# Optimization experiments

Measured on AMD Instinct MI355X. Metric: run time of the kernel, lower is better.

## Reference

```python
import jax, jax.numpy as jnp
import numpy as np

C = 64
C8 = C // 8
C16 = C // 16


def setup_inputs() -> dict:
    key = jax.random.key(0)
    ks = jax.random.split(key, 11)
    s = lambda fan_in: 1.0 / np.sqrt(fan_in)
    return {
        "x": jax.random.normal(ks[0], (4, C, 64, 64), dtype=jnp.float32),
        # 1x1 convs == per-pixel linear: weight [out, in], bias [out]
        "Wq": jax.random.uniform(ks[1], (C8, C), minval=-s(C), maxval=s(C)),
        "bq": jax.random.uniform(ks[2], (C8,), minval=-s(C), maxval=s(C)),
        "Wk": jax.random.uniform(ks[3], (C8, C), minval=-s(C), maxval=s(C)),
        "bk": jax.random.uniform(ks[4], (C8,), minval=-s(C), maxval=s(C)),
        "Wv": jax.random.uniform(ks[5], (C, C), minval=-s(C), maxval=s(C)),
        "bv": jax.random.uniform(ks[6], (C,), minval=-s(C), maxval=s(C)),
        "W1": jax.random.uniform(ks[7], (C16, C), minval=-s(C), maxval=s(C)),
        "b1": jax.random.uniform(ks[8], (C16,), minval=-s(C), maxval=s(C)),
        "W2": jax.random.uniform(ks[9], (C, C16), minval=-s(C16), maxval=s(C16)),
        "b2": jax.random.uniform(ks[10], (C,), minval=-s(C16), maxval=s(C16)),
    }


def reference(x, Wq, bq, Wk, bk, Wv, bv, W1, b1, W2, b2):
    b, c, h, w = x.shape
    n = h * w
    xf = x.reshape(b, c, n)                                   # [b,c,n]
    Q = jnp.einsum('qc,bcn->bnq', Wq, xf) + bq                # [b,n,c/8]
    K = jnp.einsum('kc,bcn->bkn', Wk, xf) + bk[None, :, None] # [b,c/8,n]
    V = jnp.einsum('vc,bcn->bvn', Wv, xf) + bv[None, :, None] # [b,c,n]
    scores = jnp.einsum('bnq,bqm->bnm', Q, K) / jnp.sqrt(jnp.float32(c))
    att = jax.nn.softmax(scores, axis=-1)                     # [b,n,n]
    # self_attention_map = V @ att^T
    sa = jnp.einsum('bvm,bnm->bvn', V, att).reshape(b, c, h, w)
    # SE-style channel gate
    avg = xf.mean(axis=2)                                     # [b,c]
    gate = jax.nn.sigmoid(jax.nn.relu(avg @ W1.T + b1) @ W2.T + b2)
    return sa * gate[:, :, None, None]
```

## Files before the change

### kernel.cpp

```cpp
#include <hip/hip_runtime.h>
#include <hip/hip_bf16.h>

typedef __attribute__((ext_vector_type(8))) short bf16x8;
typedef __attribute__((ext_vector_type(4))) float f32x4;
typedef __attribute__((ext_vector_type(4))) unsigned short u16x4;
typedef __attribute__((ext_vector_type(8))) unsigned short u16x8;

#define WS_QB 0
#define WS_KB 131072
#define WS_VB 262144
#define WS_AVG_U 1310720

__device__ __forceinline__ unsigned short bf_hi(float x) {
    __hip_bfloat16 h = __float2bfloat16(x);
    return *reinterpret_cast<unsigned short*>(&h);
}
__device__ __forceinline__ unsigned int bfpk(float lo, float hi) {
    return (unsigned int)bf_hi(lo) | ((unsigned int)bf_hi(hi) << 16);
}

__global__ __launch_bounds__(256) void proj_kernel(
    const float* __restrict__ x,
    const float* __restrict__ Wq, const float* __restrict__ bq,
    const float* __restrict__ Wk, const float* __restrict__ bk,
    const float* __restrict__ Wv, const float* __restrict__ bv,
    unsigned short* __restrict__ Qb, unsigned short* __restrict__ Kb,
    unsigned short* __restrict__ Vb, float* __restrict__ avg)
{
    __shared__ __align__(16) unsigned short Wls[16 * 72];

    const int tid = threadIdx.x;
    const int w = tid >> 6;
    const int l = tid & 63;
    const int g = l >> 4;
    const int l15 = l & 15;

    const int tile = blockIdx.x >> 8;
    const int pair = blockIdx.x & 255;
    const int b = pair >> 6;
    const int n0 = (pair & 63) << 6;
    const int n = n0 + w * 16 + l15;
    const float* xb = x + b * 262144;

    float xr[2][8];
#pragma unroll
    for (int kcb = 0; kcb < 2; ++kcb)
#pragma unroll
        for (int j = 0; j < 8; ++j)
            xr[kcb][j] = xb[(kcb * 32 + g * 8 + j) * 4096 + n];

#pragma unroll
    for (int i = 0; i < 4; ++i) {
        const int idx = i * 256 + tid;
        const int row = idx >> 6, col = idx & 63;
        float wv;
        if (tile == 0) wv = (row < 8) ? Wq[row * 64 + col] : Wk[(row - 8) * 64 + col];
        else           wv = Wv[((tile - 1) * 16 + row) * 64 + col];
        Wls[row * 72 + col] = bf_hi(wv);
    }
    __syncthreads();

    bf16x8 bfr[2];
#pragma unroll
    for (int kcb = 0; kcb < 2; ++kcb)
#pragma unroll
        for (int j = 0; j < 8; ++j)
            bfr[kcb][j] = (short)bf_hi(xr[kcb][j]);

    const bf16x8 a0 = *(const bf16x8*)&Wls[l15 * 72 + g * 8];
    const bf16x8 a1 = *(const bf16x8*)&Wls[l15 * 72 + 32 + g * 8];
    f32x4 acc;
#pragma unroll
    for (int r = 0; r < 4; ++r) acc[r] = 0.0f;
    acc = __builtin_amdgcn_mfma_f32_16x16x32_bf16(a0, bfr[0], acc, 0, 0, 0);
    acc = __builtin_amdgcn_mfma_f32_16x16x32_bf16(a1, bfr[1], acc, 0, 0, 0);

    if (tile == 0) {
        u16x4 ov;
        if (g < 2) {
#pragma unroll
            for (int r = 0; r < 4; ++r) ov[r] = bf_hi((acc[r] + bq[g * 4 + r]) * 0.125f);
            *(u16x4*)&Qb[(b * 4096 + n) * 8 + g * 4] = ov;
        } else {
#pragma unroll
            for (int r = 0; r < 4; ++r) ov[r] = bf_hi(acc[r] + bk[(g - 2) * 4 + r]);
            *(u16x4*)&Kb[(b * 4096 + n) * 8 + (g - 2) * 4] = ov;
        }
        const int c = tid >> 2;
        const float* xrow = xb + c * 4096 + n0 + ((tid & 3) << 4);
        float s = 0.0f;
#pragma unroll
        for (int k = 0; k < 4; ++k) {
            const float4 v = *(const float4*)&xrow[k * 4];
            s += (v.x + v.y) + (v.z + v.w);
        }
        s += __shfl_xor(s, 1);
        s += __shfl_xor(s, 2);
        if ((tid & 3) == 0) atomicAdd(&avg[b * 64 + c], s * (1.0f / 4096.0f));
    } else {
#pragma unroll
        for (int r = 0; r < 4; ++r) {
            const int v = (tile - 1) * 16 + g * 4 + r;
            Vb[(b * 64 + v) * 4096 + n] = bf_hi(acc[r] + bv[v]);
        }
    }
}

__global__ __launch_bounds__(512, 4) void attn_kernel(
    const unsigned short* __restrict__ Qb, const unsigned short* __restrict__ Kb,
    const unsigned short* __restrict__ Vb, const float* __restrict__ avg,
    const float* __restrict__ W1, const float* __restrict__ b1,
    const float* __restrict__ W2, const float* __restrict__ b2,
    float* __restrict__ out)
{
    __shared__ float osum[4][64][33];
    __shared__ float zls[32], gls[64], avgs[64];

    const int t = threadIdx.x;
    const int w = t >> 6;
    const int l = t & 63;
    const int g = l >> 4;
    const int l15 = l & 15;
    const int godd = g & 1;
    const int gs = (godd << 1) | (g >> 1);

    const int wg = (blockIdx.x & 7) * 64 + (blockIdx.x >> 3);
    const int b = wg >> 7;
    const int q0 = (wg & 127) << 5;

    if (t < 32) zls[t] = 0.0f;
    if (t < 64) avgs[t] = avg[b * 64 + t];
    __syncthreads();

    bf16x8 zf = {};
    bf16x8 qf[2];
#pragma unroll
    for (int qt = 0; qt < 2; ++qt) {
        bf16x8 v = *(const bf16x8*)&Qb[(b * 4096 + q0 + qt * 16 + l15) * 8];
        qf[qt] = (g == 0) ? v : zf;
    }

    const unsigned short* kb = Kb + b * 4096 * 8;
    const unsigned short* vbB = Vb + (b * 64) * 4096;

    int m0 = w * 32;
    bf16x8 kpa = zf, kpb = zf;
    if (g == 0) {
        kpa = *(const bf16x8*)&kb[(m0 + l15) * 8];
        kpb = *(const bf16x8*)&kb[(m0 + 16 + l15) * 8];
    }
    bf16x8 vp[4];
#pragma unroll
    for (int vt = 0; vt < 4; ++vt)
        vp[vt] = *(const bf16x8*)&vbB[(vt * 16 + l15) * 4096 + m0 + gs * 8];

    f32x4 acc[2][4];
#pragma unroll
    for (int qt = 0; qt < 2; ++qt)
#pragma unroll
        for (int vt = 0; vt < 4; ++vt)
#pragma unroll
            for (int r = 0; r < 4; ++r) acc[qt][vt][r] = 0.0f;
    float zreg[2] = {0.f, 0.f};

    for (int ci = 0; ci < 16; ++ci) {
        const bf16x8 ka = kpa, kc = kpb;
        bf16x8 vc[4];
#pragma unroll
        for (int vt = 0; vt < 4; ++vt) vc[vt] = vp[vt];

        const int m0n = (ci < 15) ? (w + 8 * (ci + 1)) * 32 : m0;
        if (g == 0) {
            kpa = *(const bf16x8*)&kb[(m0n + l15) * 8];
            kpb = *(const bf16x8*)&kb[(m0n + 16 + l15) * 8];
        }
#pragma unroll
        for (int vt = 0; vt < 4; ++vt)
            vp[vt] = *(const bf16x8*)&vbB[(vt * 16 + l15) * 4096 + m0n + gs * 8];

        f32x4 dz;
#pragma unroll
        for (int r = 0; r < 4; ++r) dz[r] = 0.0f;

        bf16x8 bp[2];
#pragma unroll
        for (int qt = 0; qt < 2; ++qt) {
            f32x4 d0 = __builtin_amdgcn_mfma_f32_16x16x32_bf16(ka, qf[qt], dz, 0, 0, 0);
            f32x4 d1 = __builtin_amdgcn_mfma_f32_16x16x32_bf16(kc, qf[qt], dz, 0, 0, 0);
            float p0[4], p1[4];
#pragma unroll
            for (int r = 0; r < 4; ++r) { p0[r] = __expf(d0[r]); p1[r] = __expf(d1[r]); }
            zreg[qt] += ((p0[0] + p0[1]) + (p0[2] + p0[3]))
                      + ((p1[0] + p1[1]) + (p1[2] + p1[3]));
            const unsigned int A = bfpk(p0[0], p0[1]), B = bfpk(p0[2], p0[3]);
            const unsigned int C = bfpk(p1[0], p1[1]), D = bfpk(p1[2], p1[3]);
            const unsigned int s1 = godd ? A : C;
            const unsigned int s2 = godd ? B : D;
            const unsigned int r1 = __shfl_xor(s1, 16);
            const unsigned int r2 = __shfl_xor(s2, 16);
            union { unsigned int u[4]; bf16x8 v; } pw;
            pw.u[0] = godd ? r1 : A;
            pw.u[1] = godd ? r2 : B;
            pw.u[2] = godd ? C : r1;
            pw.u[3] = godd ? D : r2;
            bp[qt] = pw.v;
        }

        __builtin_amdgcn_s_setprio(1);
#pragma unroll
        for (int vt = 0; vt < 4; ++vt) {
            acc[0][vt] = __builtin_amdgcn_mfma_f32_16x16x32_bf16(vc[vt], bp[0], acc[0][vt], 0, 0, 0);
            acc[1][vt] = __builtin_amdgcn_mfma_f32_16x16x32_bf16(vc[vt], bp[1], acc[1][vt], 0, 0, 0);
        }
        __builtin_amdgcn_s_setprio(0);
        m0 = m0n;
    }

#pragma unroll
    for (int qt = 0; qt < 2; ++qt) {
        float z = zreg[qt];
        z += __shfl_xor(z, 16);
        z += __shfl_xor(z, 32);
        if (g == 0) atomicAdd(&zls[qt * 16 + l15], z);
    }

    if (w < 4) {
#pragma unroll
        for (int qt = 0; qt < 2; ++qt)
#pragma unroll
            for (int vt = 0; vt < 4; ++vt)
#pragma unroll
                for (int r = 0; r < 4; ++r)
                    osum[w][vt * 16 + g * 4 + r][qt * 16 + l15] = acc[qt][vt][r];
    }
    if (t < 64) {
        float hreg[4];
#pragma unroll
        for (int j = 0; j < 4; ++j) {
            float hh = b1[j];
            for (int c = 0; c < 64; ++c) hh += W1[j * 64 + c] * avgs[c];
            hreg[j] = fmaxf(hh, 0.0f);
        }
        float gg = b2[t];
#pragma unroll
        for (int j = 0; j < 4; ++j) gg += W2[t * 4 + j] * hreg[j];
        gls[t] = 1.0f / (1.0f + __expf(-gg));
    }
    __syncthreads();

    if (w >= 4) {
#pragma unroll
        for (int qt = 0; qt < 2; ++qt)
#pragma unroll
            for (int vt = 0; vt < 4; ++vt)
#pragma unroll
                for (int r = 0; r < 4; ++r)
                    osum[w - 4][vt * 16 + g * 4 + r][qt * 16 + l15] += acc[qt][vt][r];
    }
    __syncthreads();

    {
        const int v = t >> 3;
        const int qb4 = (t & 7) * 4;
        const float gv = gls[v];
        float* orow = out + (b * 64 + v) * 4096 + q0 + qb4;
#pragma unroll
        for (int j = 0; j < 4; ++j) {
            const int q = qb4 + j;
            const float s = (osum[0][v][q] + osum[1][v][q])
                          + (osum[2][v][q] + osum[3][v][q]);
            orow[j] = s * (1.0f / zls[q]) * gv;
        }
    }
}

extern "C" void kernel_launch(void* const* d_in, const int* in_sizes, int n_in,
                              void* d_out, int out_size, void* d_ws, size_t ws_size,
                              hipStream_t stream) {
    const float* x  = (const float*)d_in[0];
    const float* Wq = (const float*)d_in[1];
    const float* bq = (const float*)d_in[2];
    const float* Wk = (const float*)d_in[3];
    const float* bk = (const float*)d_in[4];
    const float* Wv = (const float*)d_in[5];
    const float* bv = (const float*)d_in[6];
    const float* W1 = (const float*)d_in[7];
    const float* b1 = (const float*)d_in[8];
    const float* W2 = (const float*)d_in[9];
    const float* b2 = (const float*)d_in[10];

    unsigned short* wsu = (unsigned short*)d_ws;
    unsigned short* Qb = wsu + WS_QB;
    unsigned short* Kb = wsu + WS_KB;
    unsigned short* Vb = wsu + WS_VB;
    float* avg = (float*)(wsu + WS_AVG_U);
    float* out = (float*)d_out;

    hipMemsetAsync(avg, 0, 256 * sizeof(float), stream);
    proj_kernel<<<1280, 256, 0, stream>>>(x, Wq, bq, Wk, bk, Wv, bv, Qb, Kb, Vb, avg);
    attn_kernel<<<512, 512, 0, stream>>>(Qb, Kb, Vb, avg, W1, b1, W2, b2, out);
}
```

Baseline: 116.4 us.

## Switch attention to 16x16x16 MFMA with exp2 and double-buffered K/V prefetch

```diff
diff --git a/kernel.cpp b/kernel.cpp
--- a/kernel.cpp
+++ b/kernel.cpp
@@ -2,9 +2,15 @@
 #include <hip/hip_bf16.h>
 
 typedef __attribute__((ext_vector_type(8))) short bf16x8;
+typedef __attribute__((ext_vector_type(4))) short bf16x4;
 typedef __attribute__((ext_vector_type(4))) float f32x4;
 typedef __attribute__((ext_vector_type(4))) unsigned short u16x4;
 typedef __attribute__((ext_vector_type(8))) unsigned short u16x8;
+
+#define MFMA16(a, b, c) __builtin_amdgcn_mfma_f32_16x16x16bf16_1k(a, b, c, 0, 0, 0)
+#define EXP2f(x) exp2f(x)
+
+#define SCALE_Q 0.18033688011112042f
 
 #define WS_QB 0
 #define WS_KB 131072
@@ -79,7 +85,7 @@
         u16x4 ov;
         if (g < 2) {
 #pragma unroll
-            for (int r = 0; r < 4; ++r) ov[r] = bf_hi((acc[r] + bq[g * 4 + r]) * 0.125f);
+            for (int r = 0; r < 4; ++r) ov[r] = bf_hi((acc[r] + bq[g * 4 + r]) * SCALE_Q);
             *(u16x4*)&Qb[(b * 4096 + n) * 8 + g * 4] = ov;
         } else {
 #pragma unroll
@@ -121,8 +127,8 @@
     const int l = t & 63;
     const int g = l >> 4;
     const int l15 = l & 15;
-    const int godd = g & 1;
-    const int gs = (godd << 1) | (g >> 1);
+    const bool gk = (g < 2);
+    const int g4 = g * 4;
 
     const int wg = (blockIdx.x & 7) * 64 + (blockIdx.x >> 3);
     const int b = wg >> 7;
@@ -132,27 +138,17 @@
     if (t < 64) avgs[t] = avg[b * 64 + t];
     __syncthreads();
 
-    bf16x8 zf = {};
-    bf16x8 qf[2];
+    const bf16x4 zf4 = {};
+    bf16x4 qf[2];
 #pragma unroll
     for (int qt = 0; qt < 2; ++qt) {
-        bf16x8 v = *(const bf16x8*)&Qb[(b * 4096 + q0 + qt * 16 + l15) * 8];
-        qf[qt] = (g == 0) ? v : zf;
+        bf16x4 v = *(const bf16x4*)&Qb[(b * 4096 + q0 + qt * 16 + l15) * 8 + g4];
+        qf[qt] = gk ? v : zf4;
     }
 
     const unsigned short* kb = Kb + b * 4096 * 8;
-    const unsigned short* vbB = Vb + (b * 64) * 4096;
-
-    int m0 = w * 32;
-    bf16x8 kpa = zf, kpb = zf;
-    if (g == 0) {
-        kpa = *(const bf16x8*)&kb[(m0 + l15) * 8];
-        kpb = *(const bf16x8*)&kb[(m0 + 16 + l15) * 8];
-    }
-    bf16x8 vp[4];
-#pragma unroll
-    for (int vt = 0; vt < 4; ++vt)
-        vp[vt] = *(const bf16x8*)&vbB[(vt * 16 + l15) * 4096 + m0 + gs * 8];
+    const unsigned short* vr0 = Vb + (b * 64 + l15) * 4096;
+    const unsigned short* vrow[4] = { vr0, vr0 + 16 * 4096, vr0 + 32 * 4096, vr0 + 48 * 4096 };
 
     f32x4 acc[2][4];
 #pragma unroll
@@ -163,57 +159,62 @@
             for (int r = 0; r < 4; ++r) acc[qt][vt][r] = 0.0f;
     float zreg[2] = {0.f, 0.f};
 
-    for (int ci = 0; ci < 16; ++ci) {
-        const bf16x8 ka = kpa, kc = kpb;
-        bf16x8 vc[4];
-#pragma unroll
-        for (int vt = 0; vt < 4; ++vt) vc[vt] = vp[vt];
-
-        const int m0n = (ci < 15) ? (w + 8 * (ci + 1)) * 32 : m0;
-        if (g == 0) {
-            kpa = *(const bf16x8*)&kb[(m0n + l15) * 8];
-            kpb = *(const bf16x8*)&kb[(m0n + 16 + l15) * 8];
-        }
-#pragma unroll
-        for (int vt = 0; vt < 4; ++vt)
-            vp[vt] = *(const bf16x8*)&vbB[(vt * 16 + l15) * 4096 + m0n + gs * 8];
-
-        f32x4 dz;
-#pragma unroll
-        for (int r = 0; r < 4; ++r) dz[r] = 0.0f;
-
-        bf16x8 bp[2];
-#pragma unroll
-        for (int qt = 0; qt < 2; ++qt) {
-            f32x4 d0 = __builtin_amdgcn_mfma_f32_16x16x32_bf16(ka, qf[qt], dz, 0, 0, 0);
-            f32x4 d1 = __builtin_amdgcn_mfma_f32_16x16x32_bf16(kc, qf[qt], dz, 0, 0, 0);
-            float p0[4], p1[4];
-#pragma unroll
-            for (int r = 0; r < 4; ++r) { p0[r] = __expf(d0[r]); p1[r] = __expf(d1[r]); }
-            zreg[qt] += ((p0[0] + p0[1]) + (p0[2] + p0[3]))
-                      + ((p1[0] + p1[1]) + (p1[2] + p1[3]));
-            const unsigned int A = bfpk(p0[0], p0[1]), B = bfpk(p0[2], p0[3]);
-            const unsigned int C = bfpk(p1[0], p1[1]), D = bfpk(p1[2], p1[3]);
-            const unsigned int s1 = godd ? A : C;
-            const unsigned int s2 = godd ? B : D;
-            const unsigned int r1 = __shfl_xor(s1, 16);
-            const unsigned int r2 = __shfl_xor(s2, 16);
-            union { unsigned int u[4]; bf16x8 v; } pw;
-            pw.u[0] = godd ? r1 : A;
-            pw.u[1] = godd ? r2 : B;
-            pw.u[2] = godd ? C : r1;
-            pw.u[3] = godd ? D : r2;
-            bp[qt] = pw.v;
-        }
-
-        __builtin_amdgcn_s_setprio(1);
-#pragma unroll
-        for (int vt = 0; vt < 4; ++vt) {
-            acc[0][vt] = __builtin_amdgcn_mfma_f32_16x16x32_bf16(vc[vt], bp[0], acc[0][vt], 0, 0, 0);
-            acc[1][vt] = __builtin_amdgcn_mfma_f32_16x16x32_bf16(vc[vt], bp[1], acc[1][vt], 0, 0, 0);
-        }
-        __builtin_amdgcn_s_setprio(0);
-        m0 = m0n;
+#define RELOAD(KP, VP, M0)                                                   \
+    {                                                                        \
+        bf16x4 kv0 = *(const bf16x4*)&kb[((M0) + l15) * 8 + g4];             \
+        bf16x4 kv1 = *(const bf16x4*)&kb[((M0) + 16 + l15) * 8 + g4];        \
+        KP[0] = gk ? kv0 : zf4;                                              \
+        KP[1] = gk ? kv1 : zf4;                                              \
+        _Pragma("unroll")                                                    \
+        for (int vt = 0; vt < 4; ++vt) {                                     \
+            VP[vt][0] = *(const bf16x4*)&vrow[vt][(M0) + g4];                \
+            VP[vt][1] = *(const bf16x4*)&vrow[vt][(M0) + 16 + g4];           \
+        }                                                                    \
+    }
+
+#define CHUNK(KP, VP)                                                        \
+    {                                                                        \
+        const f32x4 dz = {0.f, 0.f, 0.f, 0.f};                               \
+        bf16x4 pb[2][2];                                                     \
+        _Pragma("unroll")                                                    \
+        for (int mt = 0; mt < 2; ++mt) {                                     \
+            _Pragma("unroll")                                                \
+            for (int qt = 0; qt < 2; ++qt) {                                 \
+                f32x4 d = MFMA16(KP[mt], qf[qt], dz);                        \
+                float p0 = EXP2f(d[0]), p1 = EXP2f(d[1]);                    \
+                float p2 = EXP2f(d[2]), p3 = EXP2f(d[3]);                    \
+                zreg[qt] += (p0 + p1) + (p2 + p3);                           \
+                union { unsigned int u[2]; bf16x4 v; } pw;                   \
+                pw.u[0] = bfpk(p0, p1);                                      \
+                pw.u[1] = bfpk(p2, p3);                                      \
+                pb[mt][qt] = pw.v;                                           \
+            }                                                                \
+        }                                                                    \
+        _Pragma("unroll")                                                    \
+        for (int vt = 0; vt < 4; ++vt) {                                     \
+            _Pragma("unroll")                                                \
+            for (int mt = 0; mt < 2; ++mt) {                                 \
+                acc[0][vt] = MFMA16(VP[vt][mt], pb[mt][0], acc[0][vt]);      \
+                acc[1][vt] = MFMA16(VP[vt][mt], pb[mt][1], acc[1][vt]);      \
+            }                                                                \
+        }                                                                    \
+    }
+
+    bf16x4 kpA[2], kpB[2];
+    bf16x4 vpA[4][2], vpB[4][2];
+    int mA = w * 32;
+    int mB = w * 32 + 256;
+    RELOAD(kpA, vpA, mA);
+    RELOAD(kpB, vpB, mB);
+
+#pragma unroll 1
+    for (int it = 0; it < 8; ++it) {
+        CHUNK(kpA, vpA);
+        mA += 512;
+        RELOAD(kpA, vpA, mA);
+        CHUNK(kpB, vpB);
+        mB += 512;
+        RELOAD(kpB, vpB, mB);
     }
 
 #pragma unroll
@@ -231,7 +232,7 @@
             for (int vt = 0; vt < 4; ++vt)
 #pragma unroll
                 for (int r = 0; r < 4; ++r)
-                    osum[w][vt * 16 + g * 4 + r][qt * 16 + l15] = acc[qt][vt][r];
+                    osum[w][vt * 16 + g4 + r][qt * 16 + l15] = acc[qt][vt][r];
     }
     if (t < 64) {
         float hreg[4];
@@ -255,7 +256,7 @@
             for (int vt = 0; vt < 4; ++vt)
 #pragma unroll
                 for (int r = 0; r < 4; ++r)
-                    osum[w - 4][vt * 16 + g * 4 + r][qt * 16 + l15] += acc[qt][vt][r];
+                    osum[w - 4][vt * 16 + g4 + r][qt * 16 + l15] += acc[qt][vt][r];
     }
     __syncthreads();
 
@@ -272,6 +273,8 @@
             orow[j] = s * (1.0f / zls[q]) * gv;
         }
     }
+#undef RELOAD
+#undef CHUNK
 }
 
 extern "C" void kernel_launch(void* const* d_in, const int* in_sizes, int n_in,
@@ -296,7 +299,7 @@
     float* avg = (float*)(wsu + WS_AVG_U);
     float* out = (float*)d_out;
 
-    hipMemsetAsync(avg, 0, 256 * sizeof(float), stream);
+    (void)hipMemsetAsync(avg, 0, 256 * sizeof(float), stream);
     proj_kernel<<<1280, 256, 0, stream>>>(x, Wq, bq, Wk, bk, Wv, bv, Qb, Kb, Vb, avg);
     attn_kernel<<<512, 512, 0, stream>>>(Qb, Kb, Vb, avg, W1, b1, W2, b2, out);
 }
```

Result: slower. 144.8 us (+24.4%).
